# Optimization experiments

Measured on AMD Instinct MI355X. Metric: run time of the kernel, lower is better.

The kernel has to match this reference:

```python
import jax, jax.numpy as jnp
import numpy as np

E = 8   # num routed experts
K = 1   # top-k per token
D = 512   # embed_dim
I = 2048  # moe_inter_dim (= 4*D)
B, T = 2, 2048


def setup_inputs() -> dict:
    key = jax.random.key(0)
    ks = jax.random.split(key, 7)
    s = 0.02
    x = jax.random.normal(ks[0], (B, T, D), jnp.float32)
    gate_w = jax.random.normal(ks[1], (E, D), jnp.float32) * s      # TopKGate.proj.weight
    w1 = jax.random.normal(ks[2], (E, I, D), jnp.float32) * s       # Expert.w1.weight per expert
    w2 = jax.random.normal(ks[3], (E, D, I), jnp.float32) * s       # Expert.w2.weight
    w3 = jax.random.normal(ks[4], (E, I, D), jnp.float32) * s       # Expert.w3.weight
    sw1 = jax.random.normal(ks[5], (I, D), jnp.float32) * s         # shared Linear(dim -> 1*inter)
    sw2 = jax.random.normal(ks[6], (D, I), jnp.float32) * s         # shared Linear(inter -> dim)
    return {"x": x, "gate_w": gate_w, "w1": w1, "w2": w2, "w3": w3, "sw1": sw1, "sw2": sw2}


def reference(x, gate_w, w1, w2, w3, sw1, sw2):
    xf = x.reshape(-1, D)                                  # [N, D]
    # gate: logits -> topk -> softmax over selected logits
    logits = xf @ gate_w.T                                 # [N, E]
    wts, idx = jax.lax.top_k(logits, K)                    # [N, K]
    wts = jax.nn.softmax(wts, axis=-1)
    # per-token combine weight for each expert (0 if not routed) -- identical
    # math to the torch gather/scatter loop, fully vectorized over experts.
    comb = jnp.einsum('nke,nk->ne', jax.nn.one_hot(idx, E, dtype=xf.dtype), wts)  # [N, E]
    # SwiGLU experts, batched over the expert axis
    h = jax.nn.silu(jnp.einsum('nd,eid->nei', xf, w1)) * jnp.einsum('nd,eid->nei', xf, w3)  # [N, E, I]
    y = jnp.einsum('nei,edi->nd', h * comb[:, :, None], w2)  # weighted combine
    # shared expert: Linear -> GELU(exact) -> Linear
    y = y + jax.nn.gelu(xf @ sw1.T, approximate=False) @ sw2.T
    return y.reshape(x.shape)
```

## Files before the change

### kernel.cpp

```cpp
#include <hip/hip_runtime.h>
#include <hip/hip_bf16.h>
#include <math.h>

#define N_TOK 4096
#define DIM 512
#define IDIM 2048
#define NEXP 8

#define W1_ELS 8388608
#define W3_ELS 8388608
#define W2_ELS 8388608
#define SW1_ELS 1048576
#define SW2_ELS 1048576
#define CONV_ELS 27262976
#define CONV_CHUNKS 3407872
#define GATE_BLOCKS 256
#define CONV_BLOCKS 2048
#define ZERO_BLOCKS 32
#define CONV_THREADS (CONV_BLOCKS * 256)

typedef __attribute__((ext_vector_type(8))) short bf16x8;
typedef __attribute__((ext_vector_type(4))) float floatx4;

__device__ __forceinline__ short f2bf(float f) {
  unsigned int u;
  __builtin_memcpy(&u, &f, 4);
  u += 0x7fff + ((u >> 16) & 1);
  return (short)(u >> 16);
}

__device__ __forceinline__ bf16x8 ld8f(const float* __restrict__ p) {
  float4 a = *(const float4*)p;
  float4 b = *(const float4*)(p + 4);
  bf16x8 v;
  v[0] = f2bf(a.x); v[1] = f2bf(a.y); v[2] = f2bf(a.z); v[3] = f2bf(a.w);
  v[4] = f2bf(b.x); v[5] = f2bf(b.y); v[6] = f2bf(b.z); v[7] = f2bf(b.w);
  return v;
}

__device__ __forceinline__ float gelu_exactish(float v) {
  float z = fabsf(v) * 0.70710678118f;
  float tt = 1.f / (1.f + 0.3275911f * z);
  float poly = tt * (0.254829592f + tt * (-0.284496736f + tt * (1.421413741f +
               tt * (-1.453152027f + tt * 1.061405429f))));
  float er = 1.f - poly * __expf(-z * z);
  er = (v < 0.f) ? -er : er;
  return 0.5f * v * (1.f + er);
}

__device__ __forceinline__ void gll(const short* g, short* l) {
  __builtin_amdgcn_global_load_lds(
      (const __attribute__((address_space(1))) void*)g,
      (__attribute__((address_space(3))) void*)l, 16, 0, 0);
}

__global__ __launch_bounds__(256) void gate_conv_kernel(
    const float* __restrict__ x, const float* __restrict__ gw,
    short* __restrict__ xb, int* __restrict__ expert_id,
    const float* __restrict__ w1, const float* __restrict__ w3,
    const float* __restrict__ w2, const float* __restrict__ sw1,
    const float* __restrict__ sw2,
    short* __restrict__ w1b, short* __restrict__ w3b, short* __restrict__ w2b,
    short* __restrict__ sw1b, short* __restrict__ sw2b,
    float* __restrict__ out) {
  __shared__ float xs[16 * 516];
  __shared__ double ps[16][8][2];
  int t = threadIdx.x;

  if (blockIdx.x >= GATE_BLOCKS + CONV_BLOCKS) {
    float4 z4 = {0.f, 0.f, 0.f, 0.f};
    long i0 = (long)(blockIdx.x - GATE_BLOCKS - CONV_BLOCKS) * 256 + t;
    for (long i = i0; i < (long)N_TOK * DIM / 4; i += (long)ZERO_BLOCKS * 256)
      ((float4*)out)[i] = z4;
    return;
  }
  if (blockIdx.x >= GATE_BLOCKS) {
    long tidg = (long)(blockIdx.x - GATE_BLOCKS) * 256 + t;
    for (long c = tidg; c < CONV_CHUNKS; c += CONV_THREADS) {
      long i = c * 8;
      const float* src;
      short* dst;
      long off;
      if (i < W1_ELS)                          { src = w1;  dst = w1b;  off = i; }
      else if (i < 2L * W1_ELS)                { src = w3;  dst = w3b;  off = i - W1_ELS; }
      else if (i < 3L * W1_ELS)                { src = w2;  dst = w2b;  off = i - 2L * W1_ELS; }
      else if (i < 3L * W1_ELS + SW1_ELS)      { src = sw1; dst = sw1b; off = i - 3L * W1_ELS; }
      else                                     { src = sw2; dst = sw2b; off = i - 3L * W1_ELS - SW1_ELS; }
      *(bf16x8*)(dst + off) = ld8f(src + off);
    }
    return;
  }

  int tok0 = blockIdx.x * 16;
  const float* xrow = x + (long)tok0 * DIM;
  for (int i = t; i < 2048; i += 256) {
    float4 v = ((const float4*)xrow)[i];
    int row = i >> 7, c4 = i & 127;
    *(float4*)&xs[row * 516 + c4 * 4] = v;
    short4 b;
    b.x = f2bf(v.x); b.y = f2bf(v.y); b.z = f2bf(v.z); b.w = f2bf(v.w);
    *(short4*)(xb + (long)tok0 * DIM + i * 4) = b;
  }
  __syncthreads();
  int tok = t & 15, e = (t >> 4) & 7, hf = t >> 7;
  const float* xr = &xs[tok * 516 + hf * 256];
  const float* wr = gw + e * DIM + hf * 256;
  double s = 0.0;
  for (int k = 0; k < 256; k += 4) {
    float4 xv = *(const float4*)(xr + k);
    float4 wv = *(const float4*)(wr + k);
    s += (double)xv.x * wv.x + (double)xv.y * wv.y +
         (double)xv.z * wv.z + (double)xv.w * wv.w;
  }
  ps[tok][e][hf] = s;
  __syncthreads();
  if (t < 16) {
    double best = ps[t][0][0] + ps[t][0][1];
    int bi = 0;
#pragma unroll
    for (int j = 1; j < 8; j++) {
      double v = ps[t][j][0] + ps[t][j][1];
      if (v > best) { best = v; bi = j; }
    }
    expert_id[tok0 + t] = bi;
  }
}

__global__ __launch_bounds__(256) void scan_scatter(
    const int* __restrict__ expert_id, int* __restrict__ counts,
    int* __restrict__ offsets, int* __restrict__ cursors, int* __restrict__ nmeta,
    int* __restrict__ te1, int* __restrict__ tr1,
    int* __restrict__ te2, int* __restrict__ tr2, int* __restrict__ perm) {
  __shared__ int cnt[8];
  int tid = threadIdx.x;
  if (tid < 8) cnt[tid] = 0;
  __syncthreads();
  for (int t = tid; t < N_TOK; t += 256) atomicAdd(&cnt[expert_id[t]], 1);
  __syncthreads();
  if (tid == 0) {
    int acc = 0;
    for (int e = 0; e < NEXP; e++) {
      counts[e] = cnt[e];
      offsets[e] = acc;
      cursors[e] = acc;
      acc += cnt[e];
    }
    int n1 = 0;
    for (int e = 0; e < NEXP; e++)
      for (int r = 0; r < cnt[e]; r += 128) { te1[n1] = e; tr1[n1] = r; n1++; }
    for (int r = 0; r < N_TOK; r += 128) { te1[n1] = 8; tr1[n1] = r; n1++; }
    int n2 = 0;
    for (int e = 0; e < NEXP; e++)
      for (int r = 0; r < cnt[e]; r += 64) { te2[n2] = e; tr2[n2] = r; n2++; }
    nmeta[0] = n1;
    nmeta[1] = n2;
  }
  __syncthreads();
  for (int t = tid; t < N_TOK; t += 256) {
    int e = expert_id[t];
    int slot = atomicAdd(&cursors[e], 1);
    perm[slot] = t;
  }
}

__global__ __launch_bounds__(256, 4) void stage1(
    const short* __restrict__ xb, const short* __restrict__ w1b,
    const short* __restrict__ w3b, const short* __restrict__ sw1b,
    short* __restrict__ h, short* __restrict__ g,
    const int* __restrict__ counts, const int* __restrict__ offsets,
    const int* __restrict__ nmeta, const int* __restrict__ te,
    const int* __restrict__ tr, const int* __restrict__ perm) {
  __shared__ short Al[128 * 64];
  __shared__ short B1l[64 * 64];
  __shared__ short B2l[64 * 64];
  int t = blockIdx.y;
  if (t >= nmeta[0]) return;
  int e = te[t], row0 = tr[t];
  bool routed = (e < 8);
  int cnt = routed ? counts[e] : N_TOK;
  int base = routed ? offsets[e] : 0;
  int n0 = blockIdx.x * 64;
  int tid = threadIdx.x, lane = tid & 63, w = tid >> 6;
  int wm = w >> 1, wn = w & 1;
  const short* B1 = routed ? w1b + (long)e * IDIM * DIM : sw1b;
  const short* B2 = w3b + (long)e * IDIM * DIM;

  int aoff[4], lbA[4];
#pragma unroll
  for (int j = 0; j < 4; j++) {
    int c = w * 256 + j * 64 + lane;
    int row = c >> 3, klog = (c & 7) ^ (row & 7);
    int srow = row0 + row;
    int slot = base + ((srow < cnt) ? srow : (cnt - 1));
    aoff[j] = perm[slot] * DIM + klog * 8;
    lbA[j] = (w * 256 + j * 64) * 8;
  }
  int bgoff[2], lbB[2];
#pragma unroll
  for (int i = 0; i < 2; i++) {
    int c = i * 256 + tid;
    int row = c >> 3, klog = (c & 7) ^ (row & 7);
    bgoff[i] = (n0 + row) * DIM + klog * 8;
    lbB[i] = (i * 256 + w * 64) * 8;
  }

  floatx4 acc[2][4][2];
#pragma unroll
  for (int m = 0; m < 2; m++)
#pragma unroll
    for (int i = 0; i < 4; i++)
#pragma unroll
      for (int j = 0; j < 2; j++) acc[m][i][j] = (floatx4)0.f;

  for (int kc = 0; kc < DIM; kc += 64) {
#pragma unroll
    for (int j = 0; j < 4; j++) gll(xb + aoff[j] + kc, &Al[lbA[j]]);
#pragma unroll
    for (int i = 0; i < 2; i++) gll(B1 + bgoff[i] + kc, &B1l[lbB[i]]);
    if (routed) {
#pragma unroll
      for (int i = 0; i < 2; i++) gll(B2 + bgoff[i] + kc, &B2l[lbB[i]]);
    }
    __syncthreads();

#pragma unroll
    for (int kf = 0; kf < 2; kf++) {
      int kp = (kf * 4 + (lane >> 4)) ^ (lane & 7);
      bf16x8 af[4];
#pragma unroll
      for (int mf = 0; mf < 4; mf++) {
        int row = wm * 64 + mf * 16 + (lane & 15);
        af[mf] = *(const bf16x8*)&Al[row * 64 + kp * 8];
      }
#pragma unroll
      for (int nf = 0; nf < 2; nf++) {
        int col = wn * 32 + nf * 16 + (lane & 15);
        bf16x8 b1 = *(const bf16x8*)&B1l[col * 64 + kp * 8];
#pragma unroll
        for (int mf = 0; mf < 4; mf++)
          acc[0][mf][nf] = __builtin_amdgcn_mfma_f32_16x16x32_bf16(
              af[mf], b1, acc[0][mf][nf], 0, 0, 0);
        if (routed) {
          bf16x8 b2 = *(const bf16x8*)&B2l[col * 64 + kp * 8];
#pragma unroll
          for (int mf = 0; mf < 4; mf++)
            acc[1][mf][nf] = __builtin_amdgcn_mfma_f32_16x16x32_bf16(
                af[mf], b2, acc[1][mf][nf], 0, 0, 0);
        }
      }
    }
    __syncthreads();
  }

  short* S = Al;
  int quad = lane >> 4;
  short* dst = routed ? h : g;
#pragma unroll
  for (int mf = 0; mf < 4; mf++)
#pragma unroll
    for (int r = 0; r < 4; r++) {
      int lr = wm * 64 + mf * 16 + quad * 4 + r;
      int sw = ((lr >> 2) & 3) << 4;
#pragma unroll
      for (int nf = 0; nf < 2; nf++) {
        int lc = wn * 32 + nf * 16 + (lane & 15);
        float a1 = acc[0][mf][nf][r];
        short v;
        if (routed) {
          float a3 = acc[1][mf][nf][r];
          v = f2bf((a1 / (1.f + __expf(-a1))) * a3);
        } else {
          v = f2bf(gelu_exactish(a1));
        }
        S[lr * 64 + ((lc & 48) ^ sw) + (lc & 15)] = v;
      }
    }
  __syncthreads();
#pragma unroll
  for (int pass = 0; pass < 2; pass++) {
    int lr = pass * 64 + (tid >> 2);
    int srow = row0 + lr;
    if (srow < cnt) {
      int p = (tid & 3) * 16;
      int lcs = p ^ (((lr >> 2) & 3) << 4);
      bf16x8 v0 = *(const bf16x8*)&S[lr * 64 + lcs];
      bf16x8 v1 = *(const bf16x8*)&S[lr * 64 + lcs + 8];
      long ro = (long)(base + srow) * IDIM + n0 + p;
      *(bf16x8*)&dst[ro] = v0;
      *(bf16x8*)&dst[ro + 8] = v1;
    }
  }
}

__global__ __launch_bounds__(256, 8) void stage2(
    const short* __restrict__ h, const short* __restrict__ g,
    const short* __restrict__ w2b, const short* __restrict__ sw2b,
    float* __restrict__ out, const int* __restrict__ counts,
    const int* __restrict__ offsets, const int* __restrict__ nmeta,
    const int* __restrict__ te, const int* __restrict__ tr,
    const int* __restrict__ perm) {
  __shared__ short Al[64 * 64];
  __shared__ short Bl[64 * 64];
  int lid = blockIdx.x + 8 * (blockIdx.y + 72 * blockIdx.z);
  int logical = (lid & 7) * 144 + (lid >> 3);
  int z = logical / 576;
  int rem = logical - z * 576;
  int t = rem >> 3;
  int n0 = (rem & 7) * 64;
  if (t >= nmeta[1]) return;
  int e = te[t], row0 = tr[t];
  int cnt = counts[e], base = offsets[e];
  const short* As = z ? g : h;
  const short* Bs = z ? sw2b : (w2b + (long)e * DIM * IDIM);
  int tid = threadIdx.x, lane = tid & 63, w = tid >> 6;
  int wm = w >> 1, wn = w & 1;

  int aoff[2], lbA[2], bgoff[2], lbB[2];
#pragma unroll
  for (int i = 0; i < 2; i++) {
    int c = i * 256 + tid;
    int row = c >> 3, klog = (c & 7) ^ (row & 7);
    int srow = row0 + row;
    int arow = base + ((srow < cnt) ? srow : (cnt - 1));
    aoff[i] = arow * IDIM + klog * 8;
    lbA[i] = (i * 256 + w * 64) * 8;
    bgoff[i] = (n0 + row) * IDIM + klog * 8;
    lbB[i] = (i * 256 + w * 64) * 8;
  }

  floatx4 acc[2][2];
#pragma unroll
  for (int i = 0; i < 2; i++)
#pragma unroll
    for (int j = 0; j < 2; j++) acc[i][j] = (floatx4)0.f;

  for (int kc = 0; kc < IDIM; kc += 64) {
#pragma unroll
    for (int i = 0; i < 2; i++) gll(As + aoff[i] + kc, &Al[lbA[i]]);
#pragma unroll
    for (int i = 0; i < 2; i++) gll(Bs + bgoff[i] + kc, &Bl[lbB[i]]);
    __syncthreads();

#pragma unroll
    for (int kf = 0; kf < 2; kf++) {
      int kp = (kf * 4 + (lane >> 4)) ^ (lane & 7);
      bf16x8 af[2];
#pragma unroll
      for (int mf = 0; mf < 2; mf++) {
        int row = wm * 32 + mf * 16 + (lane & 15);
        af[mf] = *(const bf16x8*)&Al[row * 64 + kp * 8];
      }
#pragma unroll
      for (int nf = 0; nf < 2; nf++) {
        int col = wn * 32 + nf * 16 + (lane & 15);
        bf16x8 bv = *(const bf16x8*)&Bl[col * 64 + kp * 8];
#pragma unroll
        for (int mf = 0; mf < 2; mf++)
          acc[mf][nf] = __builtin_amdgcn_mfma_f32_16x16x32_bf16(
              af[mf], bv, acc[mf][nf], 0, 0, 0);
      }
    }
    __syncthreads();
  }

  int quad = lane >> 4;
  int colb = n0 + wn * 32 + (lane & 15);
#pragma unroll
  for (int mf = 0; mf < 2; mf++)
#pragma unroll
    for (int r = 0; r < 4; r++) {
      int srow = row0 + wm * 32 + mf * 16 + quad * 4 + r;
      if (srow >= cnt) continue;
      long ro = (long)perm[base + srow] * DIM + colb;
#pragma unroll
      for (int nf = 0; nf < 2; nf++)
        atomicAdd(&out[ro + nf * 16], acc[mf][nf][r]);
    }
}

extern "C" void kernel_launch(void* const* d_in, const int* in_sizes, int n_in,
                              void* d_out, int out_size, void* d_ws, size_t ws_size,
                              hipStream_t stream) {
  const float* x = (const float*)d_in[0];
  const float* gate_w = (const float*)d_in[1];
  const float* w1 = (const float*)d_in[2];
  const float* w2 = (const float*)d_in[3];
  const float* w3 = (const float*)d_in[4];
  const float* sw1 = (const float*)d_in[5];
  const float* sw2 = (const float*)d_in[6];
  float* out = (float*)d_out;

  char* ws = (char*)d_ws;
  int* counts = (int*)ws;
  int* offsets = counts + 8;
  int* cursors = offsets + 8;
  int* nmeta = cursors + 8;
  int* te1 = nmeta + 8;
  int* tr1 = te1 + 128;
  int* te2 = tr1 + 128;
  int* tr2 = te2 + 128;
  int* expert_id = tr2 + 128;
  int* perm = expert_id + N_TOK;
  short* xb = (short*)(ws + 65536);
  short* h = xb + (size_t)N_TOK * DIM;
  short* g = h + (size_t)N_TOK * IDIM;
  short* w1b = g + (size_t)N_TOK * IDIM;
  short* w3b = w1b + (size_t)W1_ELS;
  short* w2b = w3b + (size_t)W3_ELS;
  short* sw1b = w2b + (size_t)W2_ELS;
  short* sw2b = sw1b + (size_t)SW1_ELS;

  gate_conv_kernel<<<GATE_BLOCKS + CONV_BLOCKS + ZERO_BLOCKS, 256, 0, stream>>>(
      x, gate_w, xb, expert_id, w1, w3, w2, sw1, sw2,
      w1b, w3b, w2b, sw1b, sw2b, out);
  scan_scatter<<<1, 256, 0, stream>>>(expert_id, counts, offsets, cursors, nmeta,
                                      te1, tr1, te2, tr2, perm);
  stage1<<<dim3(IDIM / 64, 72), 256, 0, stream>>>(
      xb, w1b, w3b, sw1b, h, g, counts, offsets, nmeta, te1, tr1, perm);
  stage2<<<dim3(DIM / 64, 72, 2), 256, 0, stream>>>(
      h, g, w2b, sw2b, out, counts, offsets, nmeta, te2, tr2, perm);
}
```

Before: 261.3 us.

## Fuse shared and routed down-projections in stage2, replacing atomics and zero-fill with stores

Stage2 previously split the routed-expert and shared-expert down-projections across a z grid dimension and combined them with atomicAdd into an output that a separate set of blocks zero-filled. Now each block runs both phases back to back into one accumulator, using a narrower 32-column N tile so the block count stays the same, and writes results with plain stores. This removes the zero-fill pass and the atomic traffic. In exchange each block does twice as many K iterations, and the A tile is reloaded for every 32-column slice instead of every 64, which adds A-operand memory traffic.

```diff
diff --git a/kernel.cpp b/kernel.cpp
--- a/kernel.cpp
+++ b/kernel.cpp
@@ -16,7 +16,6 @@
 #define CONV_CHUNKS 3407872
 #define GATE_BLOCKS 256
 #define CONV_BLOCKS 2048
-#define ZERO_BLOCKS 32
 #define CONV_THREADS (CONV_BLOCKS * 256)
 
 typedef __attribute__((ext_vector_type(8))) short bf16x8;
@@ -61,19 +60,11 @@
     const float* __restrict__ w2, const float* __restrict__ sw1,
     const float* __restrict__ sw2,
     short* __restrict__ w1b, short* __restrict__ w3b, short* __restrict__ w2b,
-    short* __restrict__ sw1b, short* __restrict__ sw2b,
-    float* __restrict__ out) {
+    short* __restrict__ sw1b, short* __restrict__ sw2b) {
   __shared__ float xs[16 * 516];
   __shared__ double ps[16][8][2];
   int t = threadIdx.x;
 
-  if (blockIdx.x >= GATE_BLOCKS + CONV_BLOCKS) {
-    float4 z4 = {0.f, 0.f, 0.f, 0.f};
-    long i0 = (long)(blockIdx.x - GATE_BLOCKS - CONV_BLOCKS) * 256 + t;
-    for (long i = i0; i < (long)N_TOK * DIM / 4; i += (long)ZERO_BLOCKS * 256)
-      ((float4*)out)[i] = z4;
-    return;
-  }
   if (blockIdx.x >= GATE_BLOCKS) {
     long tidg = (long)(blockIdx.x - GATE_BLOCKS) * 256 + t;
     for (long c = tidg; c < CONV_CHUNKS; c += CONV_THREADS) {
@@ -300,22 +291,19 @@
     const int* __restrict__ te, const int* __restrict__ tr,
     const int* __restrict__ perm) {
   __shared__ short Al[64 * 64];
-  __shared__ short Bl[64 * 64];
-  int lid = blockIdx.x + 8 * (blockIdx.y + 72 * blockIdx.z);
+  __shared__ short Bl[32 * 64];
+  int lid = blockIdx.x + 16 * blockIdx.y;
   int logical = (lid & 7) * 144 + (lid >> 3);
-  int z = logical / 576;
-  int rem = logical - z * 576;
-  int t = rem >> 3;
-  int n0 = (rem & 7) * 64;
+  int t = logical >> 4;
+  int n0 = (logical & 15) * 32;
   if (t >= nmeta[1]) return;
   int e = te[t], row0 = tr[t];
   int cnt = counts[e], base = offsets[e];
-  const short* As = z ? g : h;
-  const short* Bs = z ? sw2b : (w2b + (long)e * DIM * IDIM);
+  const short* w2e = w2b + (long)e * DIM * IDIM;
   int tid = threadIdx.x, lane = tid & 63, w = tid >> 6;
   int wm = w >> 1, wn = w & 1;
 
-  int aoff[2], lbA[2], bgoff[2], lbB[2];
+  int aoff[2], lbA[2];
 #pragma unroll
   for (int i = 0; i < 2; i++) {
     int c = i * 256 + tid;
@@ -324,47 +312,44 @@
     int arow = base + ((srow < cnt) ? srow : (cnt - 1));
     aoff[i] = arow * IDIM + klog * 8;
     lbA[i] = (i * 256 + w * 64) * 8;
-    bgoff[i] = (n0 + row) * IDIM + klog * 8;
-    lbB[i] = (i * 256 + w * 64) * 8;
-  }
-
-  floatx4 acc[2][2];
-#pragma unroll
-  for (int i = 0; i < 2; i++)
-#pragma unroll
-    for (int j = 0; j < 2; j++) acc[i][j] = (floatx4)0.f;
-
-  for (int kc = 0; kc < IDIM; kc += 64) {
-#pragma unroll
-    for (int i = 0; i < 2; i++) gll(As + aoff[i] + kc, &Al[lbA[i]]);
-#pragma unroll
-    for (int i = 0; i < 2; i++) gll(Bs + bgoff[i] + kc, &Bl[lbB[i]]);
-    __syncthreads();
-
-#pragma unroll
-    for (int kf = 0; kf < 2; kf++) {
-      int kp = (kf * 4 + (lane >> 4)) ^ (lane & 7);
-      bf16x8 af[2];
-#pragma unroll
-      for (int mf = 0; mf < 2; mf++) {
-        int row = wm * 32 + mf * 16 + (lane & 15);
-        af[mf] = *(const bf16x8*)&Al[row * 64 + kp * 8];
+  }
+  int brow = tid >> 3, bklog = (tid & 7) ^ (brow & 7);
+  int bgoff = (n0 + brow) * IDIM + bklog * 8;
+  int lbB = (w * 64) * 8;
+
+  floatx4 acc[2];
+  acc[0] = (floatx4)0.f;
+  acc[1] = (floatx4)0.f;
+
+#pragma unroll
+  for (int ph = 0; ph < 2; ph++) {
+    const short* As = ph ? g : h;
+    const short* Bs = ph ? sw2b : w2e;
+    for (int kc = 0; kc < IDIM; kc += 64) {
+#pragma unroll
+      for (int i = 0; i < 2; i++) gll(As + aoff[i] + kc, &Al[lbA[i]]);
+      gll(Bs + bgoff + kc, &Bl[lbB]);
+      __syncthreads();
+
+#pragma unroll
+      for (int kf = 0; kf < 2; kf++) {
+        int kp = (kf * 4 + (lane >> 4)) ^ (lane & 7);
+        int col = wn * 16 + (lane & 15);
+        bf16x8 bv = *(const bf16x8*)&Bl[col * 64 + kp * 8];
+#pragma unroll
+        for (int mf = 0; mf < 2; mf++) {
+          int row = wm * 32 + mf * 16 + (lane & 15);
+          bf16x8 af = *(const bf16x8*)&Al[row * 64 + kp * 8];
+          acc[mf] = __builtin_amdgcn_mfma_f32_16x16x32_bf16(
+              af, bv, acc[mf], 0, 0, 0);
+        }
       }
-#pragma unroll
-      for (int nf = 0; nf < 2; nf++) {
-        int col = wn * 32 + nf * 16 + (lane & 15);
-        bf16x8 bv = *(const bf16x8*)&Bl[col * 64 + kp * 8];
-#pragma unroll
-        for (int mf = 0; mf < 2; mf++)
-          acc[mf][nf] = __builtin_amdgcn_mfma_f32_16x16x32_bf16(
-              af[mf], bv, acc[mf][nf], 0, 0, 0);
-      }
-    }
-    __syncthreads();
+      __syncthreads();
+    }
   }
 
   int quad = lane >> 4;
-  int colb = n0 + wn * 32 + (lane & 15);
+  int colb = n0 + wn * 16 + (lane & 15);
 #pragma unroll
   for (int mf = 0; mf < 2; mf++)
 #pragma unroll
@@ -372,9 +357,7 @@
       int srow = row0 + wm * 32 + mf * 16 + quad * 4 + r;
       if (srow >= cnt) continue;
       long ro = (long)perm[base + srow] * DIM + colb;
-#pragma unroll
-      for (int nf = 0; nf < 2; nf++)
-        atomicAdd(&out[ro + nf * 16], acc[mf][nf][r]);
+      out[ro] = acc[mf][r];
     }
 }
 
@@ -410,13 +393,13 @@
   short* sw1b = w2b + (size_t)W2_ELS;
   short* sw2b = sw1b + (size_t)SW1_ELS;
 
-  gate_conv_kernel<<<GATE_BLOCKS + CONV_BLOCKS + ZERO_BLOCKS, 256, 0, stream>>>(
+  gate_conv_kernel<<<GATE_BLOCKS + CONV_BLOCKS, 256, 0, stream>>>(
       x, gate_w, xb, expert_id, w1, w3, w2, sw1, sw2,
-      w1b, w3b, w2b, sw1b, sw2b, out);
+      w1b, w3b, w2b, sw1b, sw2b);
   scan_scatter<<<1, 256, 0, stream>>>(expert_id, counts, offsets, cursors, nmeta,
                                       te1, tr1, te2, tr2, perm);
   stage1<<<dim3(IDIM / 64, 72), 256, 0, stream>>>(
       xb, w1b, w3b, sw1b, h, g, counts, offsets, nmeta, te1, tr1, perm);
-  stage2<<<dim3(DIM / 64, 72, 2), 256, 0, stream>>>(
+  stage2<<<dim3(16, 72), 256, 0, stream>>>(
       h, g, w2b, sw2b, out, counts, offsets, nmeta, te2, tr2, perm);
 }
```

Result: no change. 266.2 us (+1.9%).
